# Optimization experiments

Hardware: AMD Instinct MI355X
Metric: run time of the kernel (lower is better)

## Reference

```python
import jax, jax.numpy as jnp
import numpy as np

SCALING = 2.0  # lora_alpha / r


def setup_inputs() -> dict:
    key = jax.random.key(0)
    ks = jax.random.split(key, 6)
    B, S, D_IN, D_OUT, R = 4, 4096, 4096, 4096, 32
    x = jax.random.normal(ks[0], (B, S, D_IN), dtype=jnp.float32)
    W = jax.random.normal(ks[1], (D_OUT, D_IN), dtype=jnp.float32) * 0.02
    b = jax.random.normal(ks[2], (D_OUT,), dtype=jnp.float32) * 0.02
    A = jax.random.normal(ks[3], (R, D_IN), dtype=jnp.float32) * 0.02
    B_w = jax.random.normal(ks[4], (D_OUT, R), dtype=jnp.float32) * 0.02
    # per-sample activation offsets, in [1, S]
    alora_offsets = jax.random.randint(ks[5], (B,), 1, S + 1, dtype=jnp.int32)
    return {"x": x, "alora_offsets": alora_offsets, "W": W, "b": b, "A": A, "B_w": B_w}


def reference(x, alora_offsets, W, b, A, B_w):
    # base linear: y = x @ W^T + b
    base = jnp.einsum("bsd,od->bso", x, W) + b  # [B, S, D_OUT]
    # LoRA path on full sequence (dropout is identity at inference, p=0)
    lora = jnp.einsum("bsr,or->bso", jnp.einsum("bsd,rd->bsr", x, A), B_w) * SCALING
    # per-sample tail mask: only last k = min(offset, S) positions get the LoRA update
    S = x.shape[1]
    k = jnp.minimum(alora_offsets, S)  # [B]
    pos = jnp.arange(S, dtype=jnp.int32)
    mask = pos[None, :] >= (S - k)[:, None]  # [B, S] True on the tail
    return base + jnp.where(mask[:, :, None], lora, jnp.zeros((), base.dtype))
```

## Files before the change

### kernel.cpp

```cpp
#include <hip/hip_runtime.h>
#include <hip/hip_bf16.h>

typedef __attribute__((ext_vector_type(8))) short short8;
typedef __attribute__((ext_vector_type(4))) float f32x4;

#define GLOAD_LDS16(gp, lp)                                                      \
  __builtin_amdgcn_global_load_lds(                                              \
      (const __attribute__((address_space(1))) void*)(gp),                       \
      (__attribute__((address_space(3))) void*)(lp), 16, 0, 0)

#define SBAR() asm volatile("s_barrier" ::: "memory")
#define VMC(n)                                                                   \
  do {                                                                           \
    asm volatile("s_waitcnt vmcnt(" #n ")" ::: "memory");                        \
    __builtin_amdgcn_sched_barrier(0);                                           \
  } while (0)

__device__ __forceinline__ unsigned short f2bf_rne(float f) {
  union { float f; unsigned int u; } v; v.f = f;
  unsigned int u = v.u;
  u += 0x7fffu + ((u >> 16) & 1u);
  return (unsigned short)(u >> 16);
}

__global__ void cvt_f32_bf16(const float* __restrict__ src,
                             unsigned short* __restrict__ dst, int n8) {
  int i = blockIdx.x * blockDim.x + threadIdx.x;
  int stride = gridDim.x * blockDim.x;
  const f32x4* s4 = (const f32x4*)src;
  short8* d8 = (short8*)dst;
  for (; i < n8; i += stride) {
    f32x4 a = s4[2 * i], b = s4[2 * i + 1];
    short8 o;
    o[0] = (short)f2bf_rne(a[0]); o[1] = (short)f2bf_rne(a[1]);
    o[2] = (short)f2bf_rne(a[2]); o[3] = (short)f2bf_rne(a[3]);
    o[4] = (short)f2bf_rne(b[0]); o[5] = (short)f2bf_rne(b[1]);
    o[6] = (short)f2bf_rne(b[2]); o[7] = (short)f2bf_rne(b[3]);
    d8[i] = o;
  }
}

__global__ __launch_bounds__(256) void lora_t_kernel(
    const unsigned short* __restrict__ xb,
    const unsigned short* __restrict__ Ab,
    const int* __restrict__ offs,
    unsigned short* __restrict__ T)
{
  __shared__ unsigned short xs[64 * 64];
  __shared__ unsigned short as_[32 * 64];
  const int t = threadIdx.x;
  const int m0 = blockIdx.x * 64;
  const int l = t & 63, w = t >> 6;
  const int lr = l & 15, lk = (l >> 4) * 8;
  const int arow = t >> 3, acol = (t & 7) * 8;
  f32x4 acc0 = {0, 0, 0, 0}, acc1 = {0, 0, 0, 0};
  for (int kt = 0; kt < 64; ++kt) {
    __syncthreads();
    const int kof = kt * 64 + acol;
    GLOAD_LDS16(xb + (size_t)(m0 + arow) * 4096 + kof,      (char*)xs + (arow * 64 + acol) * 2);
    GLOAD_LDS16(xb + (size_t)(m0 + 32 + arow) * 4096 + kof, (char*)xs + ((32 + arow) * 64 + acol) * 2);
    GLOAD_LDS16(Ab + (size_t)arow * 4096 + kof,             (char*)as_ + (arow * 64 + acol) * 2);
    __syncthreads();
#pragma unroll
    for (int kk = 0; kk < 2; ++kk) {
      short8 a  = *(const short8*)&xs[(w * 16 + lr) * 64 + kk * 32 + lk];
      short8 b0 = *(const short8*)&as_[lr * 64 + kk * 32 + lk];
      short8 b1 = *(const short8*)&as_[(16 + lr) * 64 + kk * 32 + lk];
      acc0 = __builtin_amdgcn_mfma_f32_16x16x32_bf16(a, b0, acc0, 0, 0, 0);
      acc1 = __builtin_amdgcn_mfma_f32_16x16x32_bf16(a, b1, acc1, 0, 0, 0);
    }
  }
  const int rowb = (l >> 4) * 4;
#pragma unroll
  for (int j = 0; j < 4; ++j) {
    int m = m0 + w * 16 + rowb + j;
    int bb = m >> 12, s = m & 4095;
    int kcut = offs[bb]; if (kcut > 4096) kcut = 4096;
    bool keep = s >= 4096 - kcut;
    T[(size_t)m * 32 + lr]      = keep ? f2bf_rne(2.0f * acc0[j]) : (unsigned short)0;
    T[(size_t)m * 32 + 16 + lr] = keep ? f2bf_rne(2.0f * acc1[j]) : (unsigned short)0;
  }
}

__global__ __launch_bounds__(512, 2) void gemm_kernel(
    const unsigned short* __restrict__ xb,
    const unsigned short* __restrict__ Wb,
    const unsigned short* __restrict__ Tm,
    const unsigned short* __restrict__ Bwb,
    const float* __restrict__ bias,
    float* __restrict__ out)
{
  constexpr int K = 4096;
  extern __shared__ char smem[];

  const int bid = blockIdx.x;
  const int swz = (bid & 7) * 128 + (bid >> 3);
  const int m0 = (swz >> 4) * 256;
  const int n0 = (swz & 15) * 256;

  const int t = threadIdx.x;
  const int l = t & 63, w = t >> 6;
  const int wqr = w >> 2;
  const int pr = (w >> 1) & 1;
  const int pc = w & 1;
  const int lr = l & 15, hi = l >> 4;
  const int e0 = (hi ^ (lr & 7)) * 8;

  const int srow = t >> 3;
  const int schunk = ((t & 7) ^ ((t >> 3) & 7)) * 8;
  const unsigned short* pA0 = xb + (size_t)(m0 + srow) * K + schunk;
  const unsigned short* pA1 = xb + (size_t)(m0 + 128 + srow) * K + schunk;
  const unsigned short* pB0 = Wb + (size_t)(n0 + srow) * K + schunk;
  const unsigned short* pB1 = Wb + (size_t)(n0 + 128 + srow) * K + schunk;
  unsigned short* sm = (unsigned short*)smem;
  const int ldst = t * 16;

#define STG(PTR, SLOT, ISB, HALF, KT)                                           \
  do {                                                                          \
    const unsigned short* g_ = (PTR) + (KT) * 64;                               \
    char* d_ = smem + (SLOT) * 65536 + (ISB) * 32768 + (HALF) * 16384 + ldst;   \
    GLOAD_LDS16(g_, d_);                                                        \
    GLOAD_LDS16(g_ + (size_t)64 * K, d_ + 8192);                                \
  } while (0)

  f32x4 acc[2][4][4];
  short8 a0f[4], a1f[4], b0f[4], b1f[4];

#define RD_A(DST, AH, KK)                                                       \
  _Pragma("unroll")                                                             \
  for (int i_ = 0; i_ < 4; ++i_)                                                \
    DST[i_] = *(const short8*)((AH) + (pr * 64 + i_ * 16 + lr) * 64 + (e0 ^ ((KK) * 32)));

#define RD_B(DST, BH, KK)                                                       \
  _Pragma("unroll")                                                             \
  for (int j_ = 0; j_ < 4; ++j_)                                                \
    DST[j_] = *(const short8*)((BH) + (pc * 64 + j_ * 16 + lr) * 64 + (e0 ^ ((KK) * 32)));

#define MFMA16(QC, AF, BF)                                                      \
  _Pragma("unroll")                                                             \
  for (int i_ = 0; i_ < 4; ++i_)                                                \
    _Pragma("unroll")                                                           \
    for (int j_ = 0; j_ < 4; ++j_)                                              \
      acc[QC][i_][j_] = __builtin_amdgcn_mfma_f32_16x16x32_bf16(                \
          (AF)[i_], (BF)[j_], acc[QC][i_][j_], 0, 0, 0);

  {
    const unsigned short* tp = Tm + (size_t)(m0 + wqr * 128 + pr * 64 + lr) * 32 + hi * 8;
    short8 la[4];
#pragma unroll
    for (int i = 0; i < 4; ++i) la[i] = *(const short8*)(tp + i * 512);
    short8 lb[2][4];
#pragma unroll
    for (int qc = 0; qc < 2; ++qc)
#pragma unroll
      for (int j = 0; j < 4; ++j)
        lb[qc][j] = *(const short8*)(Bwb + (size_t)(n0 + qc * 128 + pc * 64 + j * 16 + lr) * 32 + hi * 8);
#pragma unroll
    for (int qc = 0; qc < 2; ++qc)
#pragma unroll
      for (int i = 0; i < 4; ++i)
#pragma unroll
        for (int j = 0; j < 4; ++j)
          acc[qc][i][j] = __builtin_amdgcn_mfma_f32_16x16x32_bf16(
              la[i], lb[qc][j], (f32x4){0.f, 0.f, 0.f, 0.f}, 0, 0, 0);
  }

  STG(pA0, 0, 0, 0, 0);
  STG(pA1, 0, 0, 1, 0);
  STG(pB0, 0, 1, 0, 0);
  STG(pB1, 0, 1, 1, 0);
  STG(pB0, 1, 1, 0, 1);
  VMC(2);
  SBAR();

#define WINDOW(SLOT, S0, S1, S2, S3, W0, W1, W2, W3)                            \
  {                                                                             \
    const unsigned short* Ah  = sm + (SLOT) * 32768 + wqr * 8192;               \
    const unsigned short* B0h = sm + (SLOT) * 32768 + 16384;                    \
    const unsigned short* B1h = sm + (SLOT) * 32768 + 16384 + 8192;             \
    RD_A(a0f, Ah, 0); RD_B(b0f, B0h, 0);                \
                                                             \
    RD_B(b1f, B1h, 0);                                                          \
    S0; SBAR();                                                                 \
    __builtin_amdgcn_s_setprio(1); MFMA16(0, a0f, b0f);                         \
    __builtin_amdgcn_s_setprio(0); W0; SBAR();                                  \
                                                             \
    RD_A(a1f, Ah, 1); RD_B(b0f, B0h, 1);                                        \
    S1; SBAR();                                                                 \
    __builtin_amdgcn_s_setprio(1); MFMA16(1, a0f, b1f);                         \
    __builtin_amdgcn_s_setprio(0); W1; SBAR();                                  \
                                                             \
    RD_B(b1f, B1h, 1);                                                          \
    S2; SBAR();                                                                 \
    __builtin_amdgcn_s_setprio(1); MFMA16(0, a1f, b0f);                         \
    __builtin_amdgcn_s_setprio(0); W2; SBAR();                                  \
                                                             \
    S3; SBAR();                                                                 \
    __builtin_amdgcn_s_setprio(1); MFMA16(1, a1f, b1f);                         \
    __builtin_amdgcn_s_setprio(0); W3; SBAR();                                  \
  }

  for (int I = 0; I < 31; ++I) {
    const int a = 2 * I;
    WINDOW(0, STG(pA0, 1, 0, 0, a + 1), STG(pA1, 1, 0, 1, a + 1),
              STG(pB1, 1, 1, 1, a + 1), STG(pB0, 0, 1, 0, a + 2),
              VMC(4), VMC(4), VMC(4), VMC(2));
    WINDOW(1, STG(pA0, 0, 0, 0, a + 2), STG(pA1, 0, 0, 1, a + 2),
              STG(pB1, 0, 1, 1, a + 2), STG(pB0, 1, 1, 0, a + 3),
              VMC(4), VMC(4), VMC(4), VMC(2));
  }
  WINDOW(0, STG(pA0, 1, 0, 0, 63), STG(pA1, 1, 0, 1, 63),
            STG(pB1, 1, 1, 1, 63), ((void)0),
            VMC(4), VMC(4), VMC(2), VMC(0));
  WINDOW(1, ((void)0), ((void)0), ((void)0), ((void)0),
            ((void)0), ((void)0), ((void)0), ((void)0));
#undef WINDOW
#undef MFMA16
#undef RD_A
#undef RD_B
#undef STG

  float bv[2][4];
#pragma unroll
  for (int qc = 0; qc < 2; ++qc)
#pragma unroll
    for (int j = 0; j < 4; ++j)
      bv[qc][j] = bias[n0 + qc * 128 + pc * 64 + j * 16 + lr];
  const int rowb = hi * 4;
#pragma unroll
  for (int qc = 0; qc < 2; ++qc)
#pragma unroll
    for (int i = 0; i < 4; ++i)
#pragma unroll
      for (int e = 0; e < 4; ++e) {
        int row = m0 + wqr * 128 + pr * 64 + i * 16 + rowb + e;
        float* orow = out + (size_t)row * 4096 + n0 + qc * 128 + pc * 64;
#pragma unroll
        for (int j = 0; j < 4; ++j) orow[j * 16 + lr] = acc[qc][i][j][e] + bv[qc][j];
      }
}

extern "C" void kernel_launch(void* const* d_in, const int* in_sizes, int n_in,
                              void* d_out, int out_size, void* d_ws, size_t ws_size,
                              hipStream_t stream) {
  const float* x   = (const float*)d_in[0];
  const int* offs  = (const int*)d_in[1];
  const float* W   = (const float*)d_in[2];
  const float* b   = (const float*)d_in[3];
  const float* A   = (const float*)d_in[4];
  const float* Bw  = (const float*)d_in[5];
  float* out = (float*)d_out;

  char* ws = (char*)d_ws;
  unsigned short* xb  = (unsigned short*)ws;
  unsigned short* Wb  = (unsigned short*)(ws + 134217728);
  unsigned short* Ab  = (unsigned short*)(ws + 167772160);
  unsigned short* Bwb = (unsigned short*)(ws + 168034304);
  unsigned short* T   = (unsigned short*)(ws + 168296448);

  hipFuncSetAttribute((const void*)gemm_kernel,
                      hipFuncAttributeMaxDynamicSharedMemorySize, 131072);

  cvt_f32_bf16<<<2048, 256, 0, stream>>>(x, xb, 67108864 / 8);
  cvt_f32_bf16<<<2048, 256, 0, stream>>>(W, Wb, 16777216 / 8);
  cvt_f32_bf16<<<64, 256, 0, stream>>>(A, Ab, 131072 / 8);
  cvt_f32_bf16<<<64, 256, 0, stream>>>(Bw, Bwb, 131072 / 8);
  lora_t_kernel<<<256, 256, 0, stream>>>(xb, Ab, offs, T);
  gemm_kernel<<<1024, 512, 131072, stream>>>(xb, Wb, T, Bwb, b, out);
}
```

Measured before the change: 608.4 us.

## Replace fine-grained staged barriers with one barrier per K-tile double buffer

Drops the interleaved four-phase window, where each MFMA quarter was bracketed by partial vmcnt waits and two s_barriers and loads were staggered across slots. Each window now issues the full next-tile prefetch up front, reads all fragments and runs all MFMAs, then performs a single vmcnt(0) wait plus barrier. This cuts the number of barriers per tile and lets the compiler schedule LDS reads against MFMAs freely. In exchange it loses the finer load/compute staggering and uses more fragment registers, which may reduce latency hiding or occupancy.

```diff
diff --git a/kernel.cpp b/kernel.cpp
--- a/kernel.cpp
+++ b/kernel.cpp
@@ -10,10 +10,11 @@
       (__attribute__((address_space(3))) void*)(lp), 16, 0, 0)
 
 #define SBAR() asm volatile("s_barrier" ::: "memory")
-#define VMC(n)                                                                   \
+#define BOUND()                                                                  \
   do {                                                                           \
-    asm volatile("s_waitcnt vmcnt(" #n ")" ::: "memory");                        \
+    asm volatile("s_waitcnt vmcnt(0)" ::: "memory");                             \
     __builtin_amdgcn_sched_barrier(0);                                           \
+    asm volatile("s_barrier" ::: "memory");                                      \
   } while (0)
 
 __device__ __forceinline__ unsigned short f2bf_rne(float f) {
@@ -123,8 +124,15 @@
     GLOAD_LDS16(g_ + (size_t)64 * K, d_ + 8192);                                \
   } while (0)
 
+#define STG_TILE(SLOT, KT)                                                      \
+  do {                                                                          \
+    STG(pA0, SLOT, 0, 0, KT);                                                   \
+    STG(pA1, SLOT, 0, 1, KT);                                                   \
+    STG(pB0, SLOT, 1, 0, KT);                                                   \
+    STG(pB1, SLOT, 1, 1, KT);                                                   \
+  } while (0)
+
   f32x4 acc[2][4][4];
-  short8 a0f[4], a1f[4], b0f[4], b1f[4];
 
 #define RD_A(DST, AH, KK)                                                       \
   _Pragma("unroll")                                                             \
@@ -165,59 +173,43 @@
               la[i], lb[qc][j], (f32x4){0.f, 0.f, 0.f, 0.f}, 0, 0, 0);
   }
 
-  STG(pA0, 0, 0, 0, 0);
-  STG(pA1, 0, 0, 1, 0);
-  STG(pB0, 0, 1, 0, 0);
-  STG(pB1, 0, 1, 1, 0);
-  STG(pB0, 1, 1, 0, 1);
-  VMC(2);
-  SBAR();
-
-#define WINDOW(SLOT, S0, S1, S2, S3, W0, W1, W2, W3)                            \
+  STG_TILE(0, 0);
+  BOUND();
+
+#define WIN(SLOT, STG_STMT, BOUND_STMT)                                         \
   {                                                                             \
     const unsigned short* Ah  = sm + (SLOT) * 32768 + wqr * 8192;               \
     const unsigned short* B0h = sm + (SLOT) * 32768 + 16384;                    \
     const unsigned short* B1h = sm + (SLOT) * 32768 + 16384 + 8192;             \
-    RD_A(a0f, Ah, 0); RD_B(b0f, B0h, 0);                \
-                                                             \
-    RD_B(b1f, B1h, 0);                                                          \
-    S0; SBAR();                                                                 \
-    __builtin_amdgcn_s_setprio(1); MFMA16(0, a0f, b0f);                         \
-    __builtin_amdgcn_s_setprio(0); W0; SBAR();                                  \
-                                                             \
-    RD_A(a1f, Ah, 1); RD_B(b0f, B0h, 1);                                        \
-    S1; SBAR();                                                                 \
-    __builtin_amdgcn_s_setprio(1); MFMA16(1, a0f, b1f);                         \
-    __builtin_amdgcn_s_setprio(0); W1; SBAR();                                  \
-                                                             \
-    RD_B(b1f, B1h, 1);                                                          \
-    S2; SBAR();                                                                 \
-    __builtin_amdgcn_s_setprio(1); MFMA16(0, a1f, b0f);                         \
-    __builtin_amdgcn_s_setprio(0); W2; SBAR();                                  \
-                                                             \
-    S3; SBAR();                                                                 \
-    __builtin_amdgcn_s_setprio(1); MFMA16(1, a1f, b1f);                         \
-    __builtin_amdgcn_s_setprio(0); W3; SBAR();                                  \
+    STG_STMT;                                                                   \
+    short8 aA[4], aB[4], b0[4], b1[4], b2[4], b3[4];                            \
+    RD_A(aA, Ah, 0); RD_B(b0, B0h, 0);                                          \
+    RD_B(b1, B1h, 0);                                                           \
+    __builtin_amdgcn_s_setprio(1); MFMA16(0, aA, b0);                           \
+    __builtin_amdgcn_s_setprio(0);                                              \
+    RD_A(aB, Ah, 1); RD_B(b2, B0h, 1);                                          \
+    __builtin_amdgcn_s_setprio(1); MFMA16(1, aA, b1);                           \
+    __builtin_amdgcn_s_setprio(0);                                              \
+    RD_B(b3, B1h, 1);                                                           \
+    __builtin_amdgcn_s_setprio(1); MFMA16(0, aB, b2);                           \
+    __builtin_amdgcn_s_setprio(0);                                              \
+    __builtin_amdgcn_s_setprio(1); MFMA16(1, aB, b3);                           \
+    __builtin_amdgcn_s_setprio(0);                                              \
+    BOUND_STMT;                                                                 \
   }
 
   for (int I = 0; I < 31; ++I) {
     const int a = 2 * I;
-    WINDOW(0, STG(pA0, 1, 0, 0, a + 1), STG(pA1, 1, 0, 1, a + 1),
-              STG(pB1, 1, 1, 1, a + 1), STG(pB0, 0, 1, 0, a + 2),
-              VMC(4), VMC(4), VMC(4), VMC(2));
-    WINDOW(1, STG(pA0, 0, 0, 0, a + 2), STG(pA1, 0, 0, 1, a + 2),
-              STG(pB1, 0, 1, 1, a + 2), STG(pB0, 1, 1, 0, a + 3),
-              VMC(4), VMC(4), VMC(4), VMC(2));
-  }
-  WINDOW(0, STG(pA0, 1, 0, 0, 63), STG(pA1, 1, 0, 1, 63),
-            STG(pB1, 1, 1, 1, 63), ((void)0),
-            VMC(4), VMC(4), VMC(2), VMC(0));
-  WINDOW(1, ((void)0), ((void)0), ((void)0), ((void)0),
-            ((void)0), ((void)0), ((void)0), ((void)0));
-#undef WINDOW
+    WIN(0, STG_TILE(1, a + 1), BOUND());
+    WIN(1, STG_TILE(0, a + 2), BOUND());
+  }
+  WIN(0, STG_TILE(1, 63), BOUND());
+  WIN(1, ((void)0), ((void)0));
+#undef WIN
 #undef MFMA16
 #undef RD_A
 #undef RD_B
+#undef STG_TILE
 #undef STG
 
   float bv[2][4];
```

Result: no change. 611.9 us (+0.6%).
